# Optimization experiments

Hardware: AMD Instinct MI355X
Metric: run time of the kernel (lower is better)

Reference implementation:

```python
import jax, jax.numpy as jnp
import numpy as np

N = 50000   # nodes
E = 800000  # edges (before self-loops)
IN = 256    # in_dim
H = 4       # heads
C = 64      # out_dim per head
NEG_SLOPE = 0.2
BN_EPS = 1e-5


def setup_inputs() -> dict:
    key = jax.random.key(0)
    ks = jax.random.split(key, 6)
    feature = jax.random.normal(ks[0], (N, IN), jnp.float32)
    edge_index = jax.random.randint(ks[1], (2, E), 0, N, dtype=jnp.int64)
    W = jax.random.normal(ks[2], (IN, H * C), jnp.float32) * 0.05
    att_src = jax.random.normal(ks[3], (H, C), jnp.float32) * 0.1
    att_dst = jax.random.normal(ks[4], (H, C), jnp.float32) * 0.1
    bias = jnp.zeros((H * C,), jnp.float32)
    gamma = jnp.ones((H * C,), jnp.float32)
    beta = jnp.zeros((H * C,), jnp.float32)
    return {"feature": feature, "edge_index": edge_index, "W": W,
            "att_src": att_src, "att_dst": att_dst, "bias": bias,
            "gamma": gamma, "beta": beta}


def reference(feature, edge_index, W, att_src, att_dst, bias, gamma, beta):
    n = feature.shape[0]
    # linear projection -> [N, H, C]
    x = (feature @ W).reshape(n, H, C)
    # per-node attention logits [N, H]
    a_src = jnp.einsum('nhc,hc->nh', x, att_src)
    a_dst = jnp.einsum('nhc,hc->nh', x, att_dst)
    # add self loops (PyG GATConv default)
    loop = jnp.arange(n, dtype=edge_index.dtype)
    src = jnp.concatenate([edge_index[0], loop])
    dst = jnp.concatenate([edge_index[1], loop])
    # edge attention scores [E+N, H]
    e = jax.nn.leaky_relu(a_src[src] + a_dst[dst], NEG_SLOPE)
    # segment softmax over incoming edges of each dst node
    m = jax.ops.segment_max(e, dst, num_segments=n)
    ex = jnp.exp(e - m[dst])
    denom = jax.ops.segment_sum(ex, dst, num_segments=n)
    alpha = ex / denom[dst]                       # [E+N, H]
    # weighted message aggregation -> [N, H, C]
    msg = x[src] * alpha[:, :, None]
    out = jax.ops.segment_sum(msg, dst, num_segments=n)
    h = out.reshape(n, H * C) + bias
    # batchnorm over nodes (training-mode batch statistics)
    mu = jnp.mean(h, axis=0)
    var = jnp.var(h, axis=0)
    h = (h - mu) * jax.lax.rsqrt(var + BN_EPS) * gamma + beta
    # ELU activation
    h = jax.nn.elu(h)
    # residual (in_dim == out_dim * num_heads)
    return feature + h
```

## Files before the change

kernel.cpp:

```cpp
#include <hip/hip_runtime.h>

#define N_NODES 50000
#define N_EDGES 800000
#define NEG_SLOPE 0.2f
#define BN_EPS  1e-5f

#define NBLK 256
#define EDGES_PER_BLK 3125
#define NBUCKET 196

typedef short bf16x8 __attribute__((ext_vector_type(8)));
typedef float floatx4 __attribute__((ext_vector_type(4)));

__device__ inline ushort f2bf(float f) {
    union { float f; unsigned u; } v; v.f = f;
    unsigned r = v.u + 0x7fff + ((v.u >> 16) & 1);
    return (ushort)(r >> 16);
}
__device__ inline float bf2f(ushort h) {
    union { unsigned u; float f; } v; v.u = ((unsigned)h) << 16;
    return v.f;
}

__global__ __launch_bounds__(256) void count_wt_kernel(const int* __restrict__ ei,
                                                       const float* __restrict__ W,
                                                       int* __restrict__ counts,
                                                       ushort* __restrict__ Wtb)
{
    __shared__ int hist[256];
    const int t = threadIdx.x;
    const int b = blockIdx.x;
    if (b < NBLK) {
        hist[t] = 0;
        __syncthreads();
        const int e0 = b * EDGES_PER_BLK;
        for (int e = e0 + t; e < e0 + EDGES_PER_BLK; e += 256)
            atomicAdd(&hist[ei[N_EDGES + e] >> 8], 1);
        __syncthreads();
        counts[t * NBLK + b] = hist[t];
    } else {
        const int n = b - NBLK;
        Wtb[n * 256 + t] = f2bf(W[t * 256 + n]);
    }
}

__global__ __launch_bounds__(256) void sscan1_kernel(int* __restrict__ counts,
                                                     int* __restrict__ blocksum)
{
    __shared__ int sm[256];
    const int t = threadIdx.x;
    const int i = blockIdx.x * 256 + t;
    const int v = counts[i];
    sm[t] = v;
    __syncthreads();
#pragma unroll
    for (int off = 1; off < 256; off <<= 1) {
        const int u = (t >= off) ? sm[t - off] : 0;
        __syncthreads();
        sm[t] += u;
        __syncthreads();
    }
    counts[i] = sm[t] - v;
    if (t == 255) blocksum[blockIdx.x] = sm[255];
}

__global__ __launch_bounds__(256) void sscan2_kernel(const int* __restrict__ blocksum,
                                                     int* __restrict__ blockbase,
                                                     float* __restrict__ gsum,
                                                     float* __restrict__ gsumsq)
{
    __shared__ int sm[256];
    const int t = threadIdx.x;
    const int v = blocksum[t];
    sm[t] = v;
    __syncthreads();
#pragma unroll
    for (int off = 1; off < 256; off <<= 1) {
        const int u = (t >= off) ? sm[t - off] : 0;
        __syncthreads();
        sm[t] += u;
        __syncthreads();
    }
    blockbase[t] = sm[t] - v;
    gsum[t] = 0.f;
    gsumsq[t] = 0.f;
}

__global__ __launch_bounds__(256) void sscan3_kernel(int* __restrict__ counts,
                                                     const int* __restrict__ blockbase)
{
    const int i = blockIdx.x * 256 + threadIdx.x;
    counts[i] += blockbase[blockIdx.x];
}

__global__ __launch_bounds__(256) void bucket_scatter_kernel(const int* __restrict__ ei,
                                                             const int* __restrict__ counts,
                                                             int2* __restrict__ tmp)
{
    __shared__ int cursor[256];
    const int t = threadIdx.x;
    const int blk = blockIdx.x;
    cursor[t] = counts[t * NBLK + blk];
    __syncthreads();
    const int e0 = blk * EDGES_PER_BLK;
    for (int e = e0 + t; e < e0 + EDGES_PER_BLK; e += 256) {
        const int src = ei[e];
        const int dst = ei[N_EDGES + e];
        const int pos = atomicAdd(&cursor[dst >> 8], 1);
        tmp[pos] = make_int2(dst, src);
    }
}

__global__ __launch_bounds__(256) void bucket_build_kernel(const int2* __restrict__ tmp,
                                                           const int* __restrict__ counts,
                                                           int* __restrict__ offsets,
                                                           int* __restrict__ csr_src)
{
    __shared__ int hist[256];
    __shared__ int scanbuf[256];
    __shared__ int cursor[256];
    const int t = threadIdx.x;
    const int b = blockIdx.x;
    const int start = counts[b * NBLK];
    const int end   = counts[(b + 1) * NBLK];
    hist[t] = 0;
    __syncthreads();
    for (int e = start + t; e < end; e += 256)
        atomicAdd(&hist[tmp[e].x & 255], 1);
    __syncthreads();
    const int v = hist[t];
    scanbuf[t] = v;
    __syncthreads();
#pragma unroll
    for (int off = 1; off < 256; off <<= 1) {
        const int u = (t >= off) ? scanbuf[t - off] : 0;
        __syncthreads();
        scanbuf[t] += u;
        __syncthreads();
    }
    const int excl = start + scanbuf[t] - v;
    cursor[t] = excl;
    const int node = b * 256 + t;
    if (node < N_NODES) offsets[node] = excl;
    if (b == 0 && t == 0) offsets[N_NODES] = N_EDGES;
    __syncthreads();
    for (int e = start + t; e < end; e += 256) {
        const int2 p = tmp[e];
        const int pos = atomicAdd(&cursor[p.x & 255], 1);
        csr_src[pos] = p.y;
    }
}

#define LDSTRIDE 40
__global__ __launch_bounds__(256) void gemm_kernel(const float* __restrict__ A,
                                                   const ushort* __restrict__ Bt,
                                                   const float* __restrict__ att_src,
                                                   const float* __restrict__ att_dst,
                                                   ushort* __restrict__ Xb,
                                                   float* __restrict__ s,
                                                   float* __restrict__ d)
{
    __shared__ ushort As[128 * LDSTRIDE];
    __shared__ ushort Bs[128 * LDSTRIDE];
    const int tid = threadIdx.x;
    const int lane = tid & 63;
    const int wid = tid >> 6;
    const int wm = wid & 1, wn = wid >> 1;
    const int row0 = blockIdx.y * 128;
    const int col0 = blockIdx.x * 128;

    floatx4 acc[4][4] = {};

    const int lr = tid >> 2;
    const int lk = (tid & 3) * 8;

    for (int k0 = 0; k0 < 256; k0 += 32) {
#pragma unroll
        for (int r = 0; r < 2; ++r) {
            const int row = lr + r * 64;
            const int grow = row0 + row;
            union { ushort u[8]; ulonglong2 v; } cv;
            if (grow < N_NODES) {
                const float4 f0 = *(const float4*)(A + (size_t)grow * 256 + k0 + lk);
                const float4 f1 = *(const float4*)(A + (size_t)grow * 256 + k0 + lk + 4);
                cv.u[0] = f2bf(f0.x); cv.u[1] = f2bf(f0.y);
                cv.u[2] = f2bf(f0.z); cv.u[3] = f2bf(f0.w);
                cv.u[4] = f2bf(f1.x); cv.u[5] = f2bf(f1.y);
                cv.u[6] = f2bf(f1.z); cv.u[7] = f2bf(f1.w);
            } else {
                cv.v = ulonglong2{0ull, 0ull};
            }
            *(ulonglong2*)(As + row * LDSTRIDE + lk) = cv.v;
            const ulonglong2 bv = *(const ulonglong2*)(Bt + (size_t)(col0 + row) * 256 + k0 + lk);
            *(ulonglong2*)(Bs + row * LDSTRIDE + lk) = bv;
        }
        __syncthreads();
        const int quad = lane >> 4;
        const int l16 = lane & 15;
        bf16x8 afrag[4], bfrag[4];
#pragma unroll
        for (int mi = 0; mi < 4; ++mi)
            afrag[mi] = *(const bf16x8*)(As + (wm * 64 + mi * 16 + l16) * LDSTRIDE + quad * 8);
#pragma unroll
        for (int ni = 0; ni < 4; ++ni)
            bfrag[ni] = *(const bf16x8*)(Bs + (wn * 64 + ni * 16 + l16) * LDSTRIDE + quad * 8);
#pragma unroll
        for (int mi = 0; mi < 4; ++mi)
#pragma unroll
            for (int ni = 0; ni < 4; ++ni)
                acc[mi][ni] = __builtin_amdgcn_mfma_f32_16x16x32_bf16(afrag[mi], bfrag[ni], acc[mi][ni], 0, 0, 0);
        __syncthreads();
    }

    const int quad = lane >> 4;
    const int l16 = lane & 15;
    const int head = (col0 + wn * 64) >> 6;
    float as_l[4], ad_l[4];
#pragma unroll
    for (int ni = 0; ni < 4; ++ni) {
        const int ch = head * 64 + ni * 16 + l16;
        as_l[ni] = att_src[ch];
        ad_l[ni] = att_dst[ch];
    }
#pragma unroll
    for (int mi = 0; mi < 4; ++mi) {
#pragma unroll
        for (int r = 0; r < 4; ++r) {
            const int grow = row0 + wm * 64 + mi * 16 + quad * 4 + r;
            const bool ok = grow < N_NODES;
            float vs = 0.f, vd = 0.f;
            ushort4 o;
#pragma unroll
            for (int ni = 0; ni < 4; ++ni) {
                const float v = acc[mi][ni][r];
                vs += v * as_l[ni];
                vd += v * ad_l[ni];
                ((ushort*)&o)[ni] = f2bf(v);
            }
            if (ok)
                *(ushort4*)(Xb + (size_t)grow * 256 + head * 64 + l16 * 4) = o;
#pragma unroll
            for (int m = 8; m >= 1; m >>= 1) {
                vs += __shfl_xor(vs, m);
                vd += __shfl_xor(vd, m);
            }
            if (l16 == 0 && ok) {
                s[grow * 4 + head] = vs;
                d[grow * 4 + head] = vd;
            }
        }
    }
}

__global__ __launch_bounds__(256) void aggregate_kernel(const ushort* __restrict__ xb,
                                                        const float* __restrict__ s,
                                                        const float* __restrict__ d,
                                                        const int* __restrict__ offsets,
                                                        const int* __restrict__ csr_src,
                                                        ushort* __restrict__ hagg)
{
    const int wid = threadIdx.x >> 6;
    const int lane = threadIdx.x & 63;
    const int n = blockIdx.x * 4 + wid;
    if (n >= N_NODES) return;
    const int h = lane >> 4;
    const float dn = d[n * 4 + h];
    const float sn = s[n * 4 + h];
    const ushort4 xr = *(const ushort4*)(xb + (size_t)n * 256 + lane * 4);
    float eself = sn + dn;
    eself = eself >= 0.f ? eself : NEG_SLOPE * eself;
    const float pself = __expf(eself);
    float den = pself;
    float a0 = pself * bf2f(xr.x), a1 = pself * bf2f(xr.y);
    float a2 = pself * bf2f(xr.z), a3 = pself * bf2f(xr.w);
    const int e0 = offsets[n];
    const int e1 = offsets[n + 1];
    int e = e0;
    for (; e + 8 <= e1; e += 8) {
        int si[8];
        float lg[8];
        ushort4 xv[8];
#pragma unroll
        for (int j = 0; j < 8; ++j) si[j] = csr_src[e + j];
#pragma unroll
        for (int j = 0; j < 8; ++j) lg[j] = s[si[j] * 4 + h] + dn;
#pragma unroll
        for (int j = 0; j < 8; ++j)
            xv[j] = *(const ushort4*)(xb + (size_t)si[j] * 256 + lane * 4);
#pragma unroll
        for (int j = 0; j < 8; ++j) {
            float l = lg[j];
            l = l >= 0.f ? l : NEG_SLOPE * l;
            const float p = __expf(l);
            den += p;
            a0 += p * bf2f(xv[j].x);
            a1 += p * bf2f(xv[j].y);
            a2 += p * bf2f(xv[j].z);
            a3 += p * bf2f(xv[j].w);
        }
    }
    for (; e < e1; ++e) {
        const int src = csr_src[e];
        float ee = s[src * 4 + h] + dn;
        ee = ee >= 0.f ? ee : NEG_SLOPE * ee;
        const float pe = __expf(ee);
        const ushort4 xs = *(const ushort4*)(xb + (size_t)src * 256 + lane * 4);
        a0 += pe * bf2f(xs.x); a1 += pe * bf2f(xs.y);
        a2 += pe * bf2f(xs.z); a3 += pe * bf2f(xs.w);
        den += pe;
    }
    const float inv = 1.0f / den;
    ushort4 o;
    o.x = f2bf(a0 * inv); o.y = f2bf(a1 * inv);
    o.z = f2bf(a2 * inv); o.w = f2bf(a3 * inv);
    *(ushort4*)(hagg + (size_t)n * 256 + lane * 4) = o;
}

#define BN_BLOCKS 784
__global__ __launch_bounds__(256) void bn_stats_kernel(const ushort* __restrict__ hagg,
                                                       float* __restrict__ gsum,
                                                       float* __restrict__ gsumsq)
{
    const int c = threadIdx.x;
    const int r0 = blockIdx.x * 64;
    float sum = 0.f, sq = 0.f;
#pragma unroll 4
    for (int i = 0; i < 64; ++i) {
        const int r = r0 + i;
        if (r < N_NODES) {
            const float v = bf2f(hagg[(size_t)r * 256 + c]);
            sum += v;
            sq += v * v;
        }
    }
    atomicAdd(&gsum[c], sum);
    atomicAdd(&gsumsq[c], sq);
}

__global__ __launch_bounds__(256) void finalize_kernel(const float* __restrict__ feature,
                                                       const ushort* __restrict__ hagg,
                                                       const float* __restrict__ gsum,
                                                       const float* __restrict__ gsumsq,
                                                       const float* __restrict__ gamma,
                                                       const float* __restrict__ beta,
                                                       float* __restrict__ out)
{
    const int wid = threadIdx.x >> 6;
    const int lane = threadIdx.x & 63;
    const int wgid = blockIdx.x * 4 + wid;
    const int hblk = lane >> 4;
    const int l16 = lane & 15;

    float meanv[4], scalev[4], betav[4];
    int tc[4];
#pragma unroll
    for (int j = 0; j < 4; ++j) {
        const int p = lane * 4 + j;
        tc[j] = hblk * 64 + j * 16 + l16;
        const float m = gsum[p] * (1.0f / N_NODES);
        const float var = gsumsq[p] * (1.0f / N_NODES) - m * m;
        meanv[j] = m;
        scalev[j] = gamma[tc[j]] * rsqrtf(var + BN_EPS);
        betav[j] = beta[tc[j]];
    }
#pragma unroll
    for (int rr = 0; rr < 4; ++rr) {
        const int n = wgid * 4 + rr;
        const ushort4 hv = *(const ushort4*)(hagg + (size_t)n * 256 + lane * 4);
        const float hvf[4] = {bf2f(hv.x), bf2f(hv.y), bf2f(hv.z), bf2f(hv.w)};
#pragma unroll
        for (int j = 0; j < 4; ++j) {
            float r = (hvf[j] - meanv[j]) * scalev[j] + betav[j];
            r = r > 0.f ? r : expm1f(r);
            out[(size_t)n * 256 + tc[j]] = r + feature[(size_t)n * 256 + tc[j]];
        }
    }
}

extern "C" void kernel_launch(void* const* d_in, const int* in_sizes, int n_in,
                              void* d_out, int out_size, void* d_ws, size_t ws_size,
                              hipStream_t stream)
{
    const float* feature = (const float*)d_in[0];
    const int*   ei      = (const int*)d_in[1];
    const float* W       = (const float*)d_in[2];
    const float* att_src = (const float*)d_in[3];
    const float* att_dst = (const float*)d_in[4];
    const float* gamma   = (const float*)d_in[6];
    const float* beta    = (const float*)d_in[7];
    float* out = (float*)d_out;

    char* w = (char*)d_ws;
    auto carve = [&](size_t bytes) {
        char* p = w;
        w += (bytes + 255) & ~(size_t)255;
        return p;
    };
    ushort* Wtb      = (ushort*)carve((size_t)256 * 256 * 2);
    ushort* xb       = (ushort*)carve((size_t)N_NODES * 256 * 2);
    ushort* hagg     = (ushort*)carve((size_t)N_NODES * 256 * 2);
    float*  s        = (float*)carve((size_t)N_NODES * 4 * 4);
    float*  dv       = (float*)carve((size_t)N_NODES * 4 * 4);
    int*    counts   = (int*)carve((size_t)256 * NBLK * 4);
    int*    offsets  = (int*)carve((size_t)(N_NODES + 1) * 4);
    int*    csr_src  = (int*)carve((size_t)N_EDGES * 4);
    int*    blocksum = (int*)carve((size_t)256 * 4);
    int*    blockbase= (int*)carve((size_t)256 * 4);
    float*  gsum     = (float*)carve(256 * 4);
    float*  gsumsq   = (float*)carve(256 * 4);
    int2*   tmp      = (int2*)hagg;

    count_wt_kernel<<<512, 256, 0, stream>>>(ei, W, counts, Wtb);
    sscan1_kernel<<<256, 256, 0, stream>>>(counts, blocksum);
    sscan2_kernel<<<1, 256, 0, stream>>>(blocksum, blockbase, gsum, gsumsq);
    sscan3_kernel<<<256, 256, 0, stream>>>(counts, blockbase);
    bucket_scatter_kernel<<<NBLK, 256, 0, stream>>>(ei, counts, tmp);
    bucket_build_kernel<<<NBUCKET, 256, 0, stream>>>(tmp, counts, offsets, csr_src);
    gemm_kernel<<<dim3(2, 391), 256, 0, stream>>>(feature, Wtb, att_src, att_dst, xb, s, dv);
    aggregate_kernel<<<12500, 256, 0, stream>>>(xb, s, dv, offsets, csr_src, hagg);
    bn_stats_kernel<<<BN_BLOCKS, 256, 0, stream>>>(hagg, gsum, gsumsq);
    finalize_kernel<<<3125, 256, 0, stream>>>(feature, hagg, gsum, gsumsq, gamma, beta, out);
}
```

Baseline: 294.4 us.

## Use finer 64-node buckets and packed 32-bit edge records in CSR build

The CSR construction now uses 1024 coarse buckets of 64 destination nodes instead of 256 buckets of 256. Each temp edge record is packed into a single 32-bit word (src<<6 | dst&63), halving scatter traffic. The third scan pass is folded into the scatter kernel by adding blockbase there, and the second-level bucket sort gets more, smaller blocks with a 64-entry scan. The cost is a larger counts matrix (1024x256) to scan and more LDS cursors per scatter block.

```diff
diff --git a/kernel.cpp b/kernel.cpp
--- a/kernel.cpp
+++ b/kernel.cpp
@@ -5,9 +5,10 @@
 #define NEG_SLOPE 0.2f
 #define BN_EPS  1e-5f
 
-#define NBLK 256
-#define EDGES_PER_BLK 3125
-#define NBUCKET 196
+#define CHUNKS 256
+#define EDGES_PER_CHUNK 3125
+#define NCOARSE 1024
+#define NBUCKET 782
 
 typedef short bf16x8 __attribute__((ext_vector_type(8)));
 typedef float floatx4 __attribute__((ext_vector_type(4)));
@@ -27,19 +28,20 @@
                                                        int* __restrict__ counts,
                                                        ushort* __restrict__ Wtb)
 {
-    __shared__ int hist[256];
+    __shared__ int hist[NCOARSE];
     const int t = threadIdx.x;
     const int b = blockIdx.x;
-    if (b < NBLK) {
-        hist[t] = 0;
-        __syncthreads();
-        const int e0 = b * EDGES_PER_BLK;
-        for (int e = e0 + t; e < e0 + EDGES_PER_BLK; e += 256)
-            atomicAdd(&hist[ei[N_EDGES + e] >> 8], 1);
-        __syncthreads();
-        counts[t * NBLK + b] = hist[t];
+    if (b < CHUNKS) {
+        for (int j = t; j < NCOARSE; j += 256) hist[j] = 0;
+        __syncthreads();
+        const int e0 = b * EDGES_PER_CHUNK;
+        for (int e = e0 + t; e < e0 + EDGES_PER_CHUNK; e += 256)
+            atomicAdd(&hist[ei[N_EDGES + e] >> 6], 1);
+        __syncthreads();
+        for (int j = t; j < NCOARSE; j += 256)
+            counts[j * CHUNKS + b] = hist[j];
     } else {
-        const int n = b - NBLK;
+        const int n = b - CHUNKS;
         Wtb[n * 256 + t] = f2bf(W[t * 256 + n]);
     }
 }
@@ -71,8 +73,14 @@
 {
     __shared__ int sm[256];
     const int t = threadIdx.x;
-    const int v = blocksum[t];
-    sm[t] = v;
+    int v[4], loc[4], tot = 0;
+#pragma unroll
+    for (int j = 0; j < 4; ++j) {
+        v[j] = blocksum[t * 4 + j];
+        loc[j] = tot;
+        tot += v[j];
+    }
+    sm[t] = tot;
     __syncthreads();
 #pragma unroll
     for (int off = 1; off < 256; off <<= 1) {
@@ -81,73 +89,73 @@
         sm[t] += u;
         __syncthreads();
     }
-    blockbase[t] = sm[t] - v;
+    const int base = sm[t] - tot;
+#pragma unroll
+    for (int j = 0; j < 4; ++j) blockbase[t * 4 + j] = base + loc[j];
     gsum[t] = 0.f;
     gsumsq[t] = 0.f;
 }
 
-__global__ __launch_bounds__(256) void sscan3_kernel(int* __restrict__ counts,
-                                                     const int* __restrict__ blockbase)
-{
-    const int i = blockIdx.x * 256 + threadIdx.x;
-    counts[i] += blockbase[blockIdx.x];
-}
-
 __global__ __launch_bounds__(256) void bucket_scatter_kernel(const int* __restrict__ ei,
                                                              const int* __restrict__ counts,
-                                                             int2* __restrict__ tmp)
-{
-    __shared__ int cursor[256];
+                                                             const int* __restrict__ blockbase,
+                                                             uint* __restrict__ tmp)
+{
+    __shared__ int cursor[NCOARSE];
     const int t = threadIdx.x;
     const int blk = blockIdx.x;
-    cursor[t] = counts[t * NBLK + blk];
-    __syncthreads();
-    const int e0 = blk * EDGES_PER_BLK;
-    for (int e = e0 + t; e < e0 + EDGES_PER_BLK; e += 256) {
+    for (int u = t; u < NCOARSE; u += 256)
+        cursor[u] = counts[u * CHUNKS + blk] + blockbase[u];
+    __syncthreads();
+    const int e0 = blk * EDGES_PER_CHUNK;
+    for (int e = e0 + t; e < e0 + EDGES_PER_CHUNK; e += 256) {
         const int src = ei[e];
         const int dst = ei[N_EDGES + e];
-        const int pos = atomicAdd(&cursor[dst >> 8], 1);
-        tmp[pos] = make_int2(dst, src);
-    }
-}
-
-__global__ __launch_bounds__(256) void bucket_build_kernel(const int2* __restrict__ tmp,
-                                                           const int* __restrict__ counts,
+        const int pos = atomicAdd(&cursor[dst >> 6], 1);
+        tmp[pos] = ((uint)src << 6) | (uint)(dst & 63);
+    }
+}
+
+__global__ __launch_bounds__(256) void bucket_build_kernel(const uint* __restrict__ tmp,
+                                                           const int* __restrict__ blockbase,
                                                            int* __restrict__ offsets,
                                                            int* __restrict__ csr_src)
 {
-    __shared__ int hist[256];
-    __shared__ int scanbuf[256];
-    __shared__ int cursor[256];
+    __shared__ int hist[64];
+    __shared__ int sbuf[64];
+    __shared__ int cursor[64];
     const int t = threadIdx.x;
     const int b = blockIdx.x;
-    const int start = counts[b * NBLK];
-    const int end   = counts[(b + 1) * NBLK];
-    hist[t] = 0;
+    const int start = blockbase[b];
+    const int end   = blockbase[b + 1];
+    if (t < 64) hist[t] = 0;
     __syncthreads();
     for (int e = start + t; e < end; e += 256)
-        atomicAdd(&hist[tmp[e].x & 255], 1);
-    __syncthreads();
-    const int v = hist[t];
-    scanbuf[t] = v;
-    __syncthreads();
-#pragma unroll
-    for (int off = 1; off < 256; off <<= 1) {
-        const int u = (t >= off) ? scanbuf[t - off] : 0;
-        __syncthreads();
-        scanbuf[t] += u;
-        __syncthreads();
-    }
-    const int excl = start + scanbuf[t] - v;
-    cursor[t] = excl;
-    const int node = b * 256 + t;
-    if (node < N_NODES) offsets[node] = excl;
+        atomicAdd(&hist[tmp[e] & 63], 1);
+    __syncthreads();
+    const int v = (t < 64) ? hist[t] : 0;
+    if (t < 64) sbuf[t] = v;
+    __syncthreads();
+#pragma unroll
+    for (int off = 1; off < 64; off <<= 1) {
+        int u = 0;
+        if (t < 64 && t >= off) u = sbuf[t - off];
+        __syncthreads();
+        if (t < 64) sbuf[t] += u;
+        __syncthreads();
+    }
+    if (t < 64) {
+        const int excl = start + sbuf[t] - v;
+        cursor[t] = excl;
+        const int node = b * 64 + t;
+        if (node < N_NODES) offsets[node] = excl;
+    }
     if (b == 0 && t == 0) offsets[N_NODES] = N_EDGES;
     __syncthreads();
     for (int e = start + t; e < end; e += 256) {
-        const int2 p = tmp[e];
-        const int pos = atomicAdd(&cursor[p.x & 255], 1);
-        csr_src[pos] = p.y;
+        const uint p = tmp[e];
+        const int pos = atomicAdd(&cursor[p & 63], 1);
+        csr_src[pos] = (int)(p >> 6);
     }
 }
 
@@ -401,21 +409,20 @@
     ushort* hagg     = (ushort*)carve((size_t)N_NODES * 256 * 2);
     float*  s        = (float*)carve((size_t)N_NODES * 4 * 4);
     float*  dv       = (float*)carve((size_t)N_NODES * 4 * 4);
-    int*    counts   = (int*)carve((size_t)256 * NBLK * 4);
+    int*    counts   = (int*)carve((size_t)NCOARSE * CHUNKS * 4);
     int*    offsets  = (int*)carve((size_t)(N_NODES + 1) * 4);
     int*    csr_src  = (int*)carve((size_t)N_EDGES * 4);
-    int*    blocksum = (int*)carve((size_t)256 * 4);
-    int*    blockbase= (int*)carve((size_t)256 * 4);
+    int*    blocksum = (int*)carve((size_t)NCOARSE * 4);
+    int*    blockbase= (int*)carve((size_t)NCOARSE * 4);
     float*  gsum     = (float*)carve(256 * 4);
     float*  gsumsq   = (float*)carve(256 * 4);
-    int2*   tmp      = (int2*)hagg;
+    uint*   tmp      = (uint*)hagg;
 
     count_wt_kernel<<<512, 256, 0, stream>>>(ei, W, counts, Wtb);
-    sscan1_kernel<<<256, 256, 0, stream>>>(counts, blocksum);
+    sscan1_kernel<<<NCOARSE, 256, 0, stream>>>(counts, blocksum);
     sscan2_kernel<<<1, 256, 0, stream>>>(blocksum, blockbase, gsum, gsumsq);
-    sscan3_kernel<<<256, 256, 0, stream>>>(counts, blockbase);
-    bucket_scatter_kernel<<<NBLK, 256, 0, stream>>>(ei, counts, tmp);
-    bucket_build_kernel<<<NBUCKET, 256, 0, stream>>>(tmp, counts, offsets, csr_src);
+    bucket_scatter_kernel<<<CHUNKS, 256, 0, stream>>>(ei, counts, blockbase, tmp);
+    bucket_build_kernel<<<NBUCKET, 256, 0, stream>>>(tmp, blockbase, offsets, csr_src);
     gemm_kernel<<<dim3(2, 391), 256, 0, stream>>>(feature, Wtb, att_src, att_dst, xb, s, dv);
     aggregate_kernel<<<12500, 256, 0, stream>>>(xb, s, dv, offsets, csr_src, hagg);
     bn_stats_kernel<<<BN_BLOCKS, 256, 0, stream>>>(hagg, gsum, gsumsq);
```

After: 288.6 us. 2.0% less time.
